# Kernel tuning notes

Measured on AMD Instinct MI355X. Metric: run time of the kernel, lower is better.

## Reference

```python
import jax, jax.numpy as jnp
import numpy as np

HEADS = 8
DIM_HEAD = 64
SCALE = DIM_HEAD ** -0.5


def setup_inputs() -> dict:
    key = jax.random.key(0)
    ks = jax.random.split(key, 5)
    B, N, M, D = 8, 1024, 1024, 512
    inner = HEADS * DIM_HEAD  # 512
    return {
        "x": jax.random.normal(ks[0], (B, N, D), dtype=jnp.float32),
        "context": jax.random.normal(ks[1], (B, M, D), dtype=jnp.float32),
        "Wq": jax.random.normal(ks[2], (D, inner), dtype=jnp.float32) * (D ** -0.5),
        "Wkv": jax.random.normal(ks[3], (D, 2 * inner), dtype=jnp.float32) * (D ** -0.5),
        "Wo": jax.random.normal(ks[4], (inner, D), dtype=jnp.float32) * (inner ** -0.5),
        "bo": jnp.zeros((D,), dtype=jnp.float32),
    }


def reference(x, context, Wq, Wkv, Wo, bo):
    B, N, D = x.shape
    M = context.shape[1]
    q = x @ Wq                      # [B, N, inner]
    kv = context @ Wkv              # [B, M, 2*inner]
    k, v = jnp.split(kv, 2, axis=-1)
    # b n (h d) -> b h n d
    split_heads = lambda t: t.reshape(t.shape[0], t.shape[1], HEADS, DIM_HEAD).transpose(0, 2, 1, 3)
    q, k, v = split_heads(q), split_heads(k), split_heads(v)
    dots = jnp.einsum('bhid,bhjd->bhij', q, k) * SCALE  # [B, H, N, M]
    attn = jax.nn.softmax(dots, axis=-1)
    out = jnp.einsum('bhij,bhjd->bhid', attn, v)        # [B, H, N, d]
    out = out.transpose(0, 2, 1, 3).reshape(B, N, HEADS * DIM_HEAD)
    return out @ Wo + bo            # [B, N, D]
```

## Files before the change

### kernel.cpp

```cpp
#include <hip/hip_runtime.h>
#include <stdint.h>

#define LOG2E 1.44269504088896340736f
#define QSCALE (0.125f * LOG2E)

typedef __bf16 bf16x8 __attribute__((ext_vector_type(8)));
typedef float floatx4 __attribute__((ext_vector_type(4)));

__device__ __forceinline__ unsigned short bfbits(float f) {
  __bf16 h = (__bf16)f;
  return __builtin_bit_cast(unsigned short, h);
}

__device__ __forceinline__ float fast_exp2(float x) {
#if __has_builtin(__builtin_amdgcn_exp2f)
  return __builtin_amdgcn_exp2f(x);
#else
  return exp2f(x);
#endif
}

__device__ __forceinline__ void gl2lds16(const void* g, void* l) {
  __builtin_amdgcn_global_load_lds((const __attribute__((address_space(1))) void*)g,
                                   (__attribute__((address_space(3))) void*)l, 16, 0, 0);
}

__global__ __launch_bounds__(256)
void prep_kernel(const float* __restrict__ x, const float* __restrict__ ctx,
                 const float* __restrict__ Wq, const float* __restrict__ Wkv,
                 const float* __restrict__ Wo,
                 unsigned short* __restrict__ Xb, unsigned short* __restrict__ Cb,
                 unsigned short* __restrict__ WqT, unsigned short* __restrict__ WkvT,
                 unsigned short* __restrict__ WoT) {
  int blk = blockIdx.x;
  int tid = threadIdx.x;
  if (blk < 8192) {
    const float* in = blk < 4096 ? x : ctx;
    unsigned short* out = blk < 4096 ? Xb : Cb;
    int i = (((blk & 4095) * 256) + tid) * 4;
    float4 v = *(const float4*)(in + i);
    unsigned long long pk = (unsigned long long)bfbits(v.x)
                          | ((unsigned long long)bfbits(v.y) << 16)
                          | ((unsigned long long)bfbits(v.z) << 32)
                          | ((unsigned long long)bfbits(v.w) << 48);
    *(unsigned long long*)(out + i) = pk;
  } else {
    __shared__ float tile[32][33];
    int t = blk - 8192;
    const float* in; unsigned short* out; int N; int tb;
    if (t < 256)      { in = Wq;  out = WqT;  N = 512;  tb = t; }
    else if (t < 768) { in = Wkv; out = WkvT; N = 1024; tb = t - 256; }
    else              { in = Wo;  out = WoT;  N = 512;  tb = t - 768; }
    const int K = 512;
    int nbx = N / 32;
    int n0 = (tb % nbx) * 32, k0 = (tb / nbx) * 32;
    int tx = tid & 31, ty = tid >> 5;
#pragma unroll
    for (int r = ty; r < 32; r += 8)
      tile[r][tx] = in[(long)(k0 + r) * N + n0 + tx];
    __syncthreads();
#pragma unroll
    for (int r = ty; r < 32; r += 8)
      out[(long)(n0 + r) * K + k0 + tx] = bfbits(tile[tx][r]);
  }
}

__global__ __launch_bounds__(256)
void proj_gemm(const unsigned short* __restrict__ Xb, const unsigned short* __restrict__ Cb,
               const unsigned short* __restrict__ WqT, const unsigned short* __restrict__ WkvT,
               unsigned short* __restrict__ Qb, unsigned short* __restrict__ Kb,
               unsigned short* __restrict__ Vt) {
  __shared__ unsigned short As[128 * 32];
  __shared__ unsigned short Bs[128 * 32];

  int idx = blockIdx.x;
  const unsigned short* A; const unsigned short* Bt;
  long bm, bn; int role;
  if (idx < 256) { role = 0; A = Xb; Bt = WqT;  bn = (long)(idx & 3) * 128; bm = (long)(idx >> 2) * 128; }
  else { idx -= 256; role = 1; A = Cb; Bt = WkvT; bn = (long)(idx & 7) * 128; bm = (long)(idx >> 3) * 128; }

  const int tid = threadIdx.x;
  const int wave = tid >> 6;
  const int lane = tid & 63;
  const int l15 = lane & 15;
  const int q4 = lane >> 4;
  const int wm = (wave & 1) * 64;
  const int wn = (wave >> 1) * 64;
  const int K = 512;

  floatx4 acc[4][4];
#pragma unroll
  for (int i = 0; i < 4; ++i)
#pragma unroll
    for (int j = 0; j < 4; ++j) { acc[i][j][0]=0.f; acc[i][j][1]=0.f; acc[i][j][2]=0.f; acc[i][j][3]=0.f; }

  for (int k0 = 0; k0 < K; k0 += 32) {
#pragma unroll
    for (int cc = 0; cc < 2; ++cc) {
      int c = cc * 256 + tid;
      int r = c >> 2, kc = c & 3;
      gl2lds16(A + (bm + r) * (long)K + k0 + kc * 8, (char*)As + c * 16);
      gl2lds16(Bt + (bn + r) * (long)K + k0 + kc * 8, (char*)Bs + c * 16);
    }
    __syncthreads();
    bf16x8 af[4], bfr[4];
#pragma unroll
    for (int i = 0; i < 4; ++i)
      af[i] = *(const bf16x8*)(As + (wm + i * 16 + l15) * 32 + q4 * 8);
#pragma unroll
    for (int j = 0; j < 4; ++j)
      bfr[j] = *(const bf16x8*)(Bs + (wn + j * 16 + l15) * 32 + q4 * 8);
#pragma unroll
    for (int i = 0; i < 4; ++i)
#pragma unroll
      for (int j = 0; j < 4; ++j)
        acc[i][j] = __builtin_amdgcn_mfma_f32_16x16x32_bf16(af[i], bfr[j], acc[i][j], 0, 0, 0);
    __syncthreads();
  }

  const bool vrole = (role == 1) && (bn >= 512);
#pragma unroll
  for (int i = 0; i < 4; ++i) {
#pragma unroll
    for (int j = 0; j < 4; ++j) {
      long col = bn + wn + j * 16 + l15;
      if (vrole) {
        long h = (col - 512) >> 6, d = col & 63;
        long row0 = bm + wm + i * 16 + q4 * 4;
        long b = row0 >> 10, m0 = row0 & 1023;
        unsigned long long pk = (unsigned long long)bfbits(acc[i][j][0])
                              | ((unsigned long long)bfbits(acc[i][j][1]) << 16)
                              | ((unsigned long long)bfbits(acc[i][j][2]) << 32)
                              | ((unsigned long long)bfbits(acc[i][j][3]) << 48);
        *(unsigned long long*)(Vt + ((b * 8 + h) * 64 + d) * 1024 + m0) = pk;
      } else {
        long h = col >> 6, d = col & 63;
#pragma unroll
        for (int r = 0; r < 4; ++r) {
          long row = bm + wm + i * 16 + q4 * 4 + r;
          long b = row >> 10, n = row & 1023;
          float v = acc[i][j][r];
          if (role == 0) Qb[((b * 8 + h) * 1024 + n) * 64 + d] = bfbits(v * QSCALE);
          else           Kb[((b * 8 + h) * 1024 + n) * 64 + d] = bfbits(v);
        }
      }
    }
  }
}

__global__ __launch_bounds__(256)
void attn_kernel(const unsigned short* __restrict__ Qb,
                 const unsigned short* __restrict__ Kb,
                 const unsigned short* __restrict__ Vt,
                 unsigned short* __restrict__ Ob)
{
  __shared__ unsigned short Ksm[2][4096];
  __shared__ unsigned short Vsm[2][4096];
  __shared__ unsigned short Psm[128 * 64];

  const int tid = threadIdx.x;
  const int wave = tid >> 6;
  const int lane = tid & 63;
  const int l15 = lane & 15;
  const int q4 = lane >> 4;
  const int bh = blockIdx.x;
  const int nb = blockIdx.y;

  const long qrow0 = (long)bh * 1024 + nb * 128 + wave * 32;

  bf16x8 qf[2][2];
#pragma unroll
  for (int qn = 0; qn < 2; ++qn)
#pragma unroll
    for (int ks = 0; ks < 2; ++ks)
      qf[qn][ks] = *(const bf16x8*)(Qb + (qrow0 + qn * 16 + l15) * 64 + ks * 32 + q4 * 8);

  floatx4 acc[2][4];
#pragma unroll
  for (int i = 0; i < 2; ++i)
#pragma unroll
    for (int d = 0; d < 4; ++d) { acc[i][d][0]=0.f; acc[i][d][1]=0.f; acc[i][d][2]=0.f; acc[i][d][3]=0.f; }
  float suml[2] = {0.0f, 0.0f};

  const unsigned short* Kbase = Kb + (long)bh * 65536;
  const unsigned short* Vbase = Vt + (long)bh * 65536;
  int koff[2], voff[2], lds16[2];
#pragma unroll
  for (int cc = 0; cc < 2; ++cc) {
    int c = cc * 256 + tid;
    int jrow = c >> 3;
    int cact = (c & 7) ^ (jrow & 7);
    koff[cc] = jrow * 64 + cact * 8;
    voff[cc] = jrow * 1024 + cact * 8;
    lds16[cc] = c * 16;
  }
#pragma unroll
  for (int cc = 0; cc < 2; ++cc) {
    gl2lds16(Kbase + koff[cc], (char*)Ksm[0] + lds16[cc]);
    gl2lds16(Vbase + voff[cc], (char*)Vsm[0] + lds16[cc]);
  }

  for (int t = 0; t < 16; ++t) {
    __syncthreads();
    const int cur = t & 1;
    if (t + 1 < 16) {
      const int nxt = cur ^ 1;
#pragma unroll
      for (int cc = 0; cc < 2; ++cc) {
        gl2lds16(Kbase + (t + 1) * 4096 + koff[cc], (char*)Ksm[nxt] + lds16[cc]);
        gl2lds16(Vbase + (t + 1) * 64 + voff[cc], (char*)Vsm[nxt] + lds16[cc]);
      }
    }

    floatx4 st[4][2];
#pragma unroll
    for (int jn = 0; jn < 4; ++jn)
#pragma unroll
      for (int qn = 0; qn < 2; ++qn) { st[jn][qn][0]=0.f; st[jn][qn][1]=0.f; st[jn][qn][2]=0.f; st[jn][qn][3]=0.f; }
#pragma unroll
    for (int ks = 0; ks < 2; ++ks) {
      bf16x8 kfr[4];
#pragma unroll
      for (int jn = 0; jn < 4; ++jn) {
        int j = jn * 16 + l15;
        int cact = (ks * 4 + q4) ^ (j & 7);
        kfr[jn] = *(const bf16x8*)(Ksm[cur] + j * 64 + cact * 8);
      }
#pragma unroll
      for (int jn = 0; jn < 4; ++jn)
#pragma unroll
        for (int qn = 0; qn < 2; ++qn)
          st[jn][qn] = __builtin_amdgcn_mfma_f32_16x16x32_bf16(kfr[jn], qf[qn][ks], st[jn][qn], 0, 0, 0);
    }

#pragma unroll
    for (int qn = 0; qn < 2; ++qn) {
      int prow = wave * 32 + qn * 16 + l15;
#pragma unroll
      for (int jn = 0; jn < 4; ++jn) {
        float p0 = fast_exp2(st[jn][qn][0]);
        float p1 = fast_exp2(st[jn][qn][1]);
        float p2 = fast_exp2(st[jn][qn][2]);
        float p3 = fast_exp2(st[jn][qn][3]);
        suml[qn] += (p0 + p1) + (p2 + p3);
        unsigned long long pk = (unsigned long long)bfbits(p0)
                              | ((unsigned long long)bfbits(p1) << 16)
                              | ((unsigned long long)bfbits(p2) << 32)
                              | ((unsigned long long)bfbits(p3) << 48);
        int ch16 = (jn * 2 + (q4 >> 1)) ^ (prow & 7);
        *(unsigned long long*)(Psm + prow * 64 + ch16 * 8 + (q4 & 1) * 4) = pk;
      }
    }
    __asm__ volatile("s_waitcnt lgkmcnt(0)" ::: "memory");

#pragma unroll
    for (int ks = 0; ks < 2; ++ks) {
      bf16x8 pa[2], vb[4];
#pragma unroll
      for (int i = 0; i < 2; ++i) {
        int m = wave * 32 + i * 16 + l15;
        int cact = (ks * 4 + q4) ^ (m & 7);
        pa[i] = *(const bf16x8*)(Psm + m * 64 + cact * 8);
      }
#pragma unroll
      for (int dn = 0; dn < 4; ++dn) {
        int dd = dn * 16 + l15;
        int cact = (ks * 4 + q4) ^ (dd & 7);
        vb[dn] = *(const bf16x8*)(Vsm[cur] + dd * 64 + cact * 8);
      }
#pragma unroll
      for (int i = 0; i < 2; ++i)
#pragma unroll
        for (int dn = 0; dn < 4; ++dn)
          acc[i][dn] = __builtin_amdgcn_mfma_f32_16x16x32_bf16(pa[i], vb[dn], acc[i][dn], 0, 0, 0);
    }
  }

  float inv[2], invr[2][4];
#pragma unroll
  for (int qn = 0; qn < 2; ++qn) {
    float l = suml[qn];
    l += __shfl_xor(l, 16, 64);
    l += __shfl_xor(l, 32, 64);
    inv[qn] = 1.0f / l;
#pragma unroll
    for (int r = 0; r < 4; ++r) invr[qn][r] = __shfl(inv[qn], q4 * 4 + r, 64);
  }

  const int b = bh >> 3, h = bh & 7;
#pragma unroll
  for (int i = 0; i < 2; ++i) {
#pragma unroll
    for (int dn = 0; dn < 4; ++dn) {
#pragma unroll
      for (int r = 0; r < 4; ++r) {
        long row = (long)b * 1024 + nb * 128 + wave * 32 + i * 16 + q4 * 4 + r;
        long col = h * 64 + dn * 16 + l15;
        Ob[row * 512 + col] = bfbits(acc[i][dn][r] * invr[i][r]);
      }
    }
  }
}

__global__ __launch_bounds__(256)
void out_gemm(const unsigned short* __restrict__ A,
              const unsigned short* __restrict__ Bt,
              float* __restrict__ outF, const float* __restrict__ bias) {
  __shared__ unsigned short As[64 * 32];
  __shared__ unsigned short Bs[128 * 32];

  const int tid = threadIdx.x;
  const int wave = tid >> 6;
  const int lane = tid & 63;
  const int l15 = lane & 15;
  const int q4 = lane >> 4;
  const int wm = (wave & 1) * 32;
  const int wn = (wave >> 1) * 64;
  const long bm = (long)blockIdx.y * 64;
  const long bn = (long)blockIdx.x * 128;
  const int K = 512, N = 512;

  floatx4 acc[2][4];
#pragma unroll
  for (int i = 0; i < 2; ++i)
#pragma unroll
    for (int j = 0; j < 4; ++j) { acc[i][j][0]=0.f; acc[i][j][1]=0.f; acc[i][j][2]=0.f; acc[i][j][3]=0.f; }

  for (int k0 = 0; k0 < K; k0 += 32) {
    {
      int r = tid >> 2, kc = tid & 3;
      gl2lds16(A + (bm + r) * (long)K + k0 + kc * 8, (char*)As + tid * 16);
    }
#pragma unroll
    for (int cc = 0; cc < 2; ++cc) {
      int c = cc * 256 + tid;
      int r = c >> 2, kc = c & 3;
      gl2lds16(Bt + (bn + r) * (long)K + k0 + kc * 8, (char*)Bs + c * 16);
    }
    __syncthreads();
    bf16x8 af[2], bfr[4];
#pragma unroll
    for (int i = 0; i < 2; ++i)
      af[i] = *(const bf16x8*)(As + (wm + i * 16 + l15) * 32 + q4 * 8);
#pragma unroll
    for (int j = 0; j < 4; ++j)
      bfr[j] = *(const bf16x8*)(Bs + (wn + j * 16 + l15) * 32 + q4 * 8);
#pragma unroll
    for (int i = 0; i < 2; ++i)
#pragma unroll
      for (int j = 0; j < 4; ++j)
        acc[i][j] = __builtin_amdgcn_mfma_f32_16x16x32_bf16(af[i], bfr[j], acc[i][j], 0, 0, 0);
    __syncthreads();
  }

#pragma unroll
  for (int i = 0; i < 2; ++i) {
#pragma unroll
    for (int j = 0; j < 4; ++j) {
      long col = bn + wn + j * 16 + l15;
      float bv = bias[col];
#pragma unroll
      for (int r = 0; r < 4; ++r) {
        long row = bm + wm + i * 16 + q4 * 4 + r;
        outF[row * (long)N + col] = acc[i][j][r] + bv;
      }
    }
  }
}

extern "C" void kernel_launch(void* const* d_in, const int* in_sizes, int n_in,
                              void* d_out, int out_size, void* d_ws, size_t ws_size,
                              hipStream_t stream) {
  const float* x   = (const float*)d_in[0];
  const float* ctx = (const float*)d_in[1];
  const float* Wq  = (const float*)d_in[2];
  const float* Wkv = (const float*)d_in[3];
  const float* Wo  = (const float*)d_in[4];
  const float* bo  = (const float*)d_in[5];
  float* out = (float*)d_out;

  char* ws = (char*)d_ws;
  unsigned short* Xb   = (unsigned short*)(ws);
  unsigned short* Cb   = (unsigned short*)(ws + (8u  << 20));
  unsigned short* WqT  = (unsigned short*)(ws + (16u << 20));
  unsigned short* WkvT = (unsigned short*)(ws + (17u << 20));
  unsigned short* WoT  = (unsigned short*)(ws + (19u << 20));
  unsigned short* Qb   = (unsigned short*)(ws + (20u << 20));
  unsigned short* Kb   = (unsigned short*)(ws + (28u << 20));
  unsigned short* Vt   = (unsigned short*)(ws + (36u << 20));
  unsigned short* Ob   = (unsigned short*)(ws + (44u << 20));

  prep_kernel<<<9216, 256, 0, stream>>>(x, ctx, Wq, Wkv, Wo, Xb, Cb, WqT, WkvT, WoT);
  proj_gemm<<<768, 256, 0, stream>>>(Xb, Cb, WqT, WkvT, Qb, Kb, Vt);
  attn_kernel<<<dim3(64, 8), 256, 0, stream>>>(Qb, Kb, Vt, Ob);
  out_gemm<<<dim3(4, 128), 256, 0, stream>>>(Ob, WoT, out, bo);
}
```

Measured before the change: 156.1 us.

## Split attention over key dimension into two partitions with combine kernel

Splits the key/value sequence of the attention kernel into two halves across a new grid z dimension, doubling the block count from 512 to 1024 to better fill the GPU's compute units. Each half writes unnormalized fp32 partial outputs and row sums, and a new combine kernel sums the halves, normalizes, and emits bf16. The P staging buffer is halved by processing the softmax/PV step in two phases, and launch bounds request 4 blocks per unit to raise occupancy. This adds an extra kernel launch and about 32MB of fp32 partial-output traffic. Summing the halves without a max is valid only because the kernel already omits max subtraction.

```diff
diff --git a/kernel.cpp b/kernel.cpp
--- a/kernel.cpp
+++ b/kernel.cpp
@@ -148,15 +148,16 @@
   }
 }
 
-__global__ __launch_bounds__(256)
+__global__ __launch_bounds__(256, 4)
 void attn_kernel(const unsigned short* __restrict__ Qb,
                  const unsigned short* __restrict__ Kb,
                  const unsigned short* __restrict__ Vt,
-                 unsigned short* __restrict__ Ob)
+                 float* __restrict__ Opart,
+                 float* __restrict__ Lpart)
 {
   __shared__ unsigned short Ksm[2][4096];
   __shared__ unsigned short Vsm[2][4096];
-  __shared__ unsigned short Psm[128 * 64];
+  __shared__ unsigned short Psm[128 * 32];
 
   const int tid = threadIdx.x;
   const int wave = tid >> 6;
@@ -165,6 +166,7 @@
   const int q4 = lane >> 4;
   const int bh = blockIdx.x;
   const int nb = blockIdx.y;
+  const int sp = blockIdx.z;
 
   const long qrow0 = (long)bh * 1024 + nb * 128 + wave * 32;
 
@@ -182,8 +184,8 @@
     for (int d = 0; d < 4; ++d) { acc[i][d][0]=0.f; acc[i][d][1]=0.f; acc[i][d][2]=0.f; acc[i][d][3]=0.f; }
   float suml[2] = {0.0f, 0.0f};
 
-  const unsigned short* Kbase = Kb + (long)bh * 65536;
-  const unsigned short* Vbase = Vt + (long)bh * 65536;
+  const unsigned short* Kbase = Kb + (long)bh * 65536 + sp * 8 * 4096;
+  const unsigned short* Vbase = Vt + (long)bh * 65536 + sp * 8 * 64;
   int koff[2], voff[2], lds16[2];
 #pragma unroll
   for (int cc = 0; cc < 2; ++cc) {
@@ -200,10 +202,10 @@
     gl2lds16(Vbase + voff[cc], (char*)Vsm[0] + lds16[cc]);
   }
 
-  for (int t = 0; t < 16; ++t) {
+  for (int t = 0; t < 8; ++t) {
     __syncthreads();
     const int cur = t & 1;
-    if (t + 1 < 16) {
+    if (t + 1 < 8) {
       const int nxt = cur ^ 1;
 #pragma unroll
       for (int cc = 0; cc < 2; ++cc) {
@@ -234,38 +236,39 @@
     }
 
 #pragma unroll
-    for (int qn = 0; qn < 2; ++qn) {
-      int prow = wave * 32 + qn * 16 + l15;
-#pragma unroll
-      for (int jn = 0; jn < 4; ++jn) {
-        float p0 = fast_exp2(st[jn][qn][0]);
-        float p1 = fast_exp2(st[jn][qn][1]);
-        float p2 = fast_exp2(st[jn][qn][2]);
-        float p3 = fast_exp2(st[jn][qn][3]);
-        suml[qn] += (p0 + p1) + (p2 + p3);
-        unsigned long long pk = (unsigned long long)bfbits(p0)
-                              | ((unsigned long long)bfbits(p1) << 16)
-                              | ((unsigned long long)bfbits(p2) << 32)
-                              | ((unsigned long long)bfbits(p3) << 48);
-        int ch16 = (jn * 2 + (q4 >> 1)) ^ (prow & 7);
-        *(unsigned long long*)(Psm + prow * 64 + ch16 * 8 + (q4 & 1) * 4) = pk;
-      }
-    }
-    __asm__ volatile("s_waitcnt lgkmcnt(0)" ::: "memory");
-
-#pragma unroll
-    for (int ks = 0; ks < 2; ++ks) {
+    for (int ph = 0; ph < 2; ++ph) {
+#pragma unroll
+      for (int qn = 0; qn < 2; ++qn) {
+        int prow = wave * 32 + qn * 16 + l15;
+#pragma unroll
+        for (int jj = 0; jj < 2; ++jj) {
+          int jn = ph * 2 + jj;
+          float p0 = fast_exp2(st[jn][qn][0]);
+          float p1 = fast_exp2(st[jn][qn][1]);
+          float p2 = fast_exp2(st[jn][qn][2]);
+          float p3 = fast_exp2(st[jn][qn][3]);
+          suml[qn] += (p0 + p1) + (p2 + p3);
+          unsigned long long pk = (unsigned long long)bfbits(p0)
+                                | ((unsigned long long)bfbits(p1) << 16)
+                                | ((unsigned long long)bfbits(p2) << 32)
+                                | ((unsigned long long)bfbits(p3) << 48);
+          int ch = (jj * 2 + (q4 >> 1)) ^ (prow & 3);
+          *(unsigned long long*)(Psm + prow * 32 + ch * 8 + (q4 & 1) * 4) = pk;
+        }
+      }
+      __asm__ volatile("s_waitcnt lgkmcnt(0)" ::: "memory");
+
       bf16x8 pa[2], vb[4];
 #pragma unroll
       for (int i = 0; i < 2; ++i) {
         int m = wave * 32 + i * 16 + l15;
-        int cact = (ks * 4 + q4) ^ (m & 7);
-        pa[i] = *(const bf16x8*)(Psm + m * 64 + cact * 8);
+        int cact = q4 ^ (m & 3);
+        pa[i] = *(const bf16x8*)(Psm + m * 32 + cact * 8);
       }
 #pragma unroll
       for (int dn = 0; dn < 4; ++dn) {
         int dd = dn * 16 + l15;
-        int cact = (ks * 4 + q4) ^ (dd & 7);
+        int cact = (ph * 4 + q4) ^ (dd & 7);
         vb[dn] = *(const bf16x8*)(Vsm[cur] + dd * 64 + cact * 8);
       }
 #pragma unroll
@@ -276,17 +279,16 @@
     }
   }
 
-  float inv[2], invr[2][4];
 #pragma unroll
   for (int qn = 0; qn < 2; ++qn) {
     float l = suml[qn];
     l += __shfl_xor(l, 16, 64);
     l += __shfl_xor(l, 32, 64);
-    inv[qn] = 1.0f / l;
-#pragma unroll
-    for (int r = 0; r < 4; ++r) invr[qn][r] = __shfl(inv[qn], q4 * 4 + r, 64);
-  }
-
+    if (q4 == 0)
+      Lpart[(long)sp * 65536 + (long)bh * 1024 + nb * 128 + wave * 32 + qn * 16 + l15] = l;
+  }
+
+  float* Op = Opart + (long)sp * 8192 * 512;
   const int b = bh >> 3, h = bh & 7;
 #pragma unroll
   for (int i = 0; i < 2; ++i) {
@@ -296,10 +298,31 @@
       for (int r = 0; r < 4; ++r) {
         long row = (long)b * 1024 + nb * 128 + wave * 32 + i * 16 + q4 * 4 + r;
         long col = h * 64 + dn * 16 + l15;
-        Ob[row * 512 + col] = bfbits(acc[i][dn][r] * invr[i][r]);
-      }
-    }
-  }
+        Op[row * 512 + col] = acc[i][dn][r];
+      }
+    }
+  }
+}
+
+__global__ __launch_bounds__(256)
+void combine_kernel(const float* __restrict__ Opart, const float* __restrict__ Lpart,
+                    unsigned short* __restrict__ Ob) {
+  int g = blockIdx.x * 256 + threadIdx.x;
+  int row = g >> 7;
+  int c4 = g & 127;
+  int b = row >> 10, n = row & 1023, h = c4 >> 4;
+  long lidx = (long)(b * 8 + h) * 1024 + n;
+  float l1 = Lpart[lidx];
+  float l2 = Lpart[65536 + lidx];
+  float inv = 1.0f / (l1 + l2);
+  long oidx = (long)row * 512 + c4 * 4;
+  float4 o1 = *(const float4*)(Opart + oidx);
+  float4 o2 = *(const float4*)(Opart + 8192L * 512 + oidx);
+  unsigned long long pk = (unsigned long long)bfbits((o1.x + o2.x) * inv)
+                        | ((unsigned long long)bfbits((o1.y + o2.y) * inv) << 16)
+                        | ((unsigned long long)bfbits((o1.z + o2.z) * inv) << 32)
+                        | ((unsigned long long)bfbits((o1.w + o2.w) * inv) << 48);
+  *(unsigned long long*)(Ob + oidx) = pk;
 }
 
 __global__ __launch_bounds__(256)
@@ -389,9 +412,12 @@
   unsigned short* Kb   = (unsigned short*)(ws + (28u << 20));
   unsigned short* Vt   = (unsigned short*)(ws + (36u << 20));
   unsigned short* Ob   = (unsigned short*)(ws + (44u << 20));
+  float*          Opart = (float*)(ws + (52u << 20));
+  float*          Lpart = (float*)(ws + (86u << 20));
 
   prep_kernel<<<9216, 256, 0, stream>>>(x, ctx, Wq, Wkv, Wo, Xb, Cb, WqT, WkvT, WoT);
   proj_gemm<<<768, 256, 0, stream>>>(Xb, Cb, WqT, WkvT, Qb, Kb, Vt);
-  attn_kernel<<<dim3(64, 8), 256, 0, stream>>>(Qb, Kb, Vt, Ob);
+  attn_kernel<<<dim3(64, 8, 2), 256, 0, stream>>>(Qb, Kb, Vt, Opart, Lpart);
+  combine_kernel<<<4096, 256, 0, stream>>>(Opart, Lpart, Ob);
   out_gemm<<<dim3(4, 128), 256, 0, stream>>>(Ob, WoT, out, bo);
 }
```

After: 160.7 us. +2.9%, slower.

## Software-pipeline attention loop: defer PV MFMA by one tile, overlapping with exp

Applied to the files above, without the earlier changes.

The attention inner loop now computes P·V for the previous key tile while computing exp and P stores for the current tile. To support this it triple-buffers V in LDS and double-buffers P, and adds an epilogue for the last tile. The goal is to hide the exp/pack latency and the LDS round-trip wait behind MFMA work instead of serializing them with an explicit lgkmcnt wait. Swizzled LDS offsets are also precomputed once. The cost is more LDS per block, which may reduce occupancy, and more live registers.

```diff
diff --git a/kernel.cpp b/kernel.cpp
--- a/kernel.cpp
+++ b/kernel.cpp
@@ -155,8 +155,8 @@
                  unsigned short* __restrict__ Ob)
 {
   __shared__ unsigned short Ksm[2][4096];
-  __shared__ unsigned short Vsm[2][4096];
-  __shared__ unsigned short Psm[128 * 64];
+  __shared__ unsigned short Vsm[3][4096];
+  __shared__ unsigned short Psm[2][8192];
 
   const int tid = threadIdx.x;
   const int wave = tid >> 6;
@@ -194,6 +194,24 @@
     voff[cc] = jrow * 1024 + cact * 8;
     lds16[cc] = c * 16;
   }
+
+  const int s7 = l15 & 7;
+  int kfo[2][4], pao[2][2], pwo[2][4];
+#pragma unroll
+  for (int ks = 0; ks < 2; ++ks) {
+#pragma unroll
+    for (int jn = 0; jn < 4; ++jn)
+      kfo[ks][jn] = (jn * 16 + l15) * 64 + (((ks * 4 + q4) ^ s7) * 8);
+#pragma unroll
+    for (int i = 0; i < 2; ++i)
+      pao[ks][i] = (wave * 32 + i * 16 + l15) * 64 + (((ks * 4 + q4) ^ s7) * 8);
+  }
+#pragma unroll
+  for (int qn = 0; qn < 2; ++qn)
+#pragma unroll
+    for (int jn = 0; jn < 4; ++jn)
+      pwo[qn][jn] = (wave * 32 + qn * 16 + l15) * 64 + (((jn * 2 + (q4 >> 1)) ^ s7) * 8) + (q4 & 1) * 4;
+
 #pragma unroll
   for (int cc = 0; cc < 2; ++cc) {
     gl2lds16(Kbase + koff[cc], (char*)Ksm[0] + lds16[cc]);
@@ -202,13 +220,16 @@
 
   for (int t = 0; t < 16; ++t) {
     __syncthreads();
-    const int cur = t & 1;
+    const int kc = t & 1;
     if (t + 1 < 16) {
-      const int nxt = cur ^ 1;
+      char* KL = (char*)Ksm[kc ^ 1];
+      char* VL = (char*)Vsm[(t + 1) % 3];
+      const unsigned short* Kn = Kbase + (t + 1) * 4096;
+      const unsigned short* Vn = Vbase + (t + 1) * 64;
 #pragma unroll
       for (int cc = 0; cc < 2; ++cc) {
-        gl2lds16(Kbase + (t + 1) * 4096 + koff[cc], (char*)Ksm[nxt] + lds16[cc]);
-        gl2lds16(Vbase + (t + 1) * 64 + voff[cc], (char*)Vsm[nxt] + lds16[cc]);
+        gl2lds16(Kn + koff[cc], KL + lds16[cc]);
+        gl2lds16(Vn + voff[cc], VL + lds16[cc]);
       }
     }
 
@@ -217,15 +238,13 @@
     for (int jn = 0; jn < 4; ++jn)
 #pragma unroll
       for (int qn = 0; qn < 2; ++qn) { st[jn][qn][0]=0.f; st[jn][qn][1]=0.f; st[jn][qn][2]=0.f; st[jn][qn][3]=0.f; }
+    const unsigned short* Kc = Ksm[kc];
 #pragma unroll
     for (int ks = 0; ks < 2; ++ks) {
       bf16x8 kfr[4];
 #pragma unroll
-      for (int jn = 0; jn < 4; ++jn) {
-        int j = jn * 16 + l15;
-        int cact = (ks * 4 + q4) ^ (j & 7);
-        kfr[jn] = *(const bf16x8*)(Ksm[cur] + j * 64 + cact * 8);
-      }
+      for (int jn = 0; jn < 4; ++jn)
+        kfr[jn] = *(const bf16x8*)(Kc + kfo[ks][jn]);
 #pragma unroll
       for (int jn = 0; jn < 4; ++jn)
 #pragma unroll
@@ -233,41 +252,76 @@
           st[jn][qn] = __builtin_amdgcn_mfma_f32_16x16x32_bf16(kfr[jn], qf[qn][ks], st[jn][qn], 0, 0, 0);
     }
 
-#pragma unroll
-    for (int qn = 0; qn < 2; ++qn) {
-      int prow = wave * 32 + qn * 16 + l15;
-#pragma unroll
-      for (int jn = 0; jn < 4; ++jn) {
-        float p0 = fast_exp2(st[jn][qn][0]);
-        float p1 = fast_exp2(st[jn][qn][1]);
-        float p2 = fast_exp2(st[jn][qn][2]);
-        float p3 = fast_exp2(st[jn][qn][3]);
-        suml[qn] += (p0 + p1) + (p2 + p3);
-        unsigned long long pk = (unsigned long long)bfbits(p0)
-                              | ((unsigned long long)bfbits(p1) << 16)
-                              | ((unsigned long long)bfbits(p2) << 32)
-                              | ((unsigned long long)bfbits(p3) << 48);
-        int ch16 = (jn * 2 + (q4 >> 1)) ^ (prow & 7);
-        *(unsigned long long*)(Psm + prow * 64 + ch16 * 8 + (q4 & 1) * 4) = pk;
-      }
-    }
-    __asm__ volatile("s_waitcnt lgkmcnt(0)" ::: "memory");
-
+    unsigned short* Pc = Psm[t & 1];
+    const unsigned short* Pp = Psm[(t & 1) ^ 1];
+    const unsigned short* Vp = Vsm[(t + 2) % 3];
+    const bool havePrev = (t > 0);
+
+    bf16x8 pa0[2], vb0[4];
+    if (havePrev) {
+#pragma unroll
+      for (int i = 0; i < 2; ++i) pa0[i] = *(const bf16x8*)(Pp + pao[0][i]);
+#pragma unroll
+      for (int dn = 0; dn < 4; ++dn) vb0[dn] = *(const bf16x8*)(Vp + kfo[0][dn]);
+    }
+#pragma unroll
+    for (int jn = 0; jn < 4; ++jn) {
+      float p0 = fast_exp2(st[jn][0][0]);
+      float p1 = fast_exp2(st[jn][0][1]);
+      float p2 = fast_exp2(st[jn][0][2]);
+      float p3 = fast_exp2(st[jn][0][3]);
+      suml[0] += (p0 + p1) + (p2 + p3);
+      unsigned int lo = (unsigned int)bfbits(p0) | ((unsigned int)bfbits(p1) << 16);
+      unsigned int hi = (unsigned int)bfbits(p2) | ((unsigned int)bfbits(p3) << 16);
+      unsigned long long pk = (unsigned long long)lo | ((unsigned long long)hi << 32);
+      *(unsigned long long*)(Pc + pwo[0][jn]) = pk;
+    }
+    if (havePrev) {
+#pragma unroll
+      for (int i = 0; i < 2; ++i)
+#pragma unroll
+        for (int dn = 0; dn < 4; ++dn)
+          acc[i][dn] = __builtin_amdgcn_mfma_f32_16x16x32_bf16(pa0[i], vb0[dn], acc[i][dn], 0, 0, 0);
+    }
+
+    bf16x8 pa1[2], vb1[4];
+    if (havePrev) {
+#pragma unroll
+      for (int i = 0; i < 2; ++i) pa1[i] = *(const bf16x8*)(Pp + pao[1][i]);
+#pragma unroll
+      for (int dn = 0; dn < 4; ++dn) vb1[dn] = *(const bf16x8*)(Vp + kfo[1][dn]);
+    }
+#pragma unroll
+    for (int jn = 0; jn < 4; ++jn) {
+      float p0 = fast_exp2(st[jn][1][0]);
+      float p1 = fast_exp2(st[jn][1][1]);
+      float p2 = fast_exp2(st[jn][1][2]);
+      float p3 = fast_exp2(st[jn][1][3]);
+      suml[1] += (p0 + p1) + (p2 + p3);
+      unsigned int lo = (unsigned int)bfbits(p0) | ((unsigned int)bfbits(p1) << 16);
+      unsigned int hi = (unsigned int)bfbits(p2) | ((unsigned int)bfbits(p3) << 16);
+      unsigned long long pk = (unsigned long long)lo | ((unsigned long long)hi << 32);
+      *(unsigned long long*)(Pc + pwo[1][jn]) = pk;
+    }
+    if (havePrev) {
+#pragma unroll
+      for (int i = 0; i < 2; ++i)
+#pragma unroll
+        for (int dn = 0; dn < 4; ++dn)
+          acc[i][dn] = __builtin_amdgcn_mfma_f32_16x16x32_bf16(pa1[i], vb1[dn], acc[i][dn], 0, 0, 0);
+    }
+  }
+
+  {
+    const unsigned short* Pp = Psm[1];
+    const unsigned short* Vp = Vsm[15 % 3];
 #pragma unroll
     for (int ks = 0; ks < 2; ++ks) {
       bf16x8 pa[2], vb[4];
 #pragma unroll
-      for (int i = 0; i < 2; ++i) {
-        int m = wave * 32 + i * 16 + l15;
-        int cact = (ks * 4 + q4) ^ (m & 7);
-        pa[i] = *(const bf16x8*)(Psm + m * 64 + cact * 8);
-      }
-#pragma unroll
-      for (int dn = 0; dn < 4; ++dn) {
-        int dd = dn * 16 + l15;
-        int cact = (ks * 4 + q4) ^ (dd & 7);
-        vb[dn] = *(const bf16x8*)(Vsm[cur] + dd * 64 + cact * 8);
-      }
+      for (int i = 0; i < 2; ++i) pa[i] = *(const bf16x8*)(Pp + pao[ks][i]);
+#pragma unroll
+      for (int dn = 0; dn < 4; ++dn) vb[dn] = *(const bf16x8*)(Vp + kfo[ks][dn]);
 #pragma unroll
       for (int i = 0; i < 2; ++i)
 #pragma unroll
```

Measured after the change: 156.6 us. No clear change (+0.3%).

## Double KV tile to 128 keys per iteration and precompute LDS offsets

Applied to the files above, without the earlier changes.

The attention inner loop now handles 128 keys per step instead of 64, halving the iteration count and the number of block barriers. K and V LDS buffers double in size, and V uses a 16-way XOR swizzle to match the wider rows. P is written and consumed in two 64-key phases so the P buffer stays the same size. Fragment and store offsets are hoisted into precomputed arrays. This raises LDS use to about 80KB per block and adds register pressure from 16 score accumulators, which may lower occupancy.

```diff
diff --git a/kernel.cpp b/kernel.cpp
--- a/kernel.cpp
+++ b/kernel.cpp
@@ -154,9 +154,9 @@
                  const unsigned short* __restrict__ Vt,
                  unsigned short* __restrict__ Ob)
 {
-  __shared__ unsigned short Ksm[2][4096];
-  __shared__ unsigned short Vsm[2][4096];
-  __shared__ unsigned short Psm[128 * 64];
+  __shared__ unsigned short Ksm[2][8192];
+  __shared__ unsigned short Vsm[2][8192];
+  __shared__ unsigned short Psm[8192];
 
   const int tid = threadIdx.x;
   const int wave = tid >> 6;
@@ -184,95 +184,122 @@
 
   const unsigned short* Kbase = Kb + (long)bh * 65536;
   const unsigned short* Vbase = Vt + (long)bh * 65536;
-  int koff[2], voff[2], lds16[2];
-#pragma unroll
-  for (int cc = 0; cc < 2; ++cc) {
+  int koff[4], voff[4], lds16[4];
+#pragma unroll
+  for (int cc = 0; cc < 4; ++cc) {
     int c = cc * 256 + tid;
-    int jrow = c >> 3;
-    int cact = (c & 7) ^ (jrow & 7);
-    koff[cc] = jrow * 64 + cact * 8;
-    voff[cc] = jrow * 1024 + cact * 8;
+    int kr = c >> 3;
+    int kcact = (c & 7) ^ (kr & 7);
+    koff[cc] = kr * 64 + kcact * 8;
+    int vr = c >> 4;
+    int vcact = (c & 15) ^ (vr & 15);
+    voff[cc] = vr * 1024 + vcact * 8;
     lds16[cc] = c * 16;
   }
-#pragma unroll
-  for (int cc = 0; cc < 2; ++cc) {
+
+  const int s7 = l15 & 7;
+  int kfo[2][8];
+#pragma unroll
+  for (int ks = 0; ks < 2; ++ks)
+#pragma unroll
+    for (int jn = 0; jn < 8; ++jn)
+      kfo[ks][jn] = (jn * 16 + l15) * 64 + (((ks * 4 + q4) ^ s7) * 8);
+  int vfo[2][2][4];
+#pragma unroll
+  for (int ph = 0; ph < 2; ++ph)
+#pragma unroll
+    for (int ks = 0; ks < 2; ++ks)
+#pragma unroll
+      for (int dn = 0; dn < 4; ++dn) {
+        int r = dn * 16 + l15;
+        vfo[ph][ks][dn] = r * 128 + (((ph * 8 + ks * 4 + q4) ^ (r & 15)) * 8);
+      }
+  int pao[2][2], pwo[2][4];
+#pragma unroll
+  for (int ks = 0; ks < 2; ++ks)
+#pragma unroll
+    for (int i = 0; i < 2; ++i)
+      pao[ks][i] = (wave * 32 + i * 16 + l15) * 64 + (((ks * 4 + q4) ^ s7) * 8);
+#pragma unroll
+  for (int qn = 0; qn < 2; ++qn)
+#pragma unroll
+    for (int jl = 0; jl < 4; ++jl)
+      pwo[qn][jl] = (wave * 32 + qn * 16 + l15) * 64 + (((jl * 2 + (q4 >> 1)) ^ s7) * 8) + (q4 & 1) * 4;
+
+#pragma unroll
+  for (int cc = 0; cc < 4; ++cc) {
     gl2lds16(Kbase + koff[cc], (char*)Ksm[0] + lds16[cc]);
     gl2lds16(Vbase + voff[cc], (char*)Vsm[0] + lds16[cc]);
   }
 
-  for (int t = 0; t < 16; ++t) {
+  for (int t = 0; t < 8; ++t) {
     __syncthreads();
     const int cur = t & 1;
-    if (t + 1 < 16) {
+    if (t + 1 < 8) {
       const int nxt = cur ^ 1;
-#pragma unroll
-      for (int cc = 0; cc < 2; ++cc) {
-        gl2lds16(Kbase + (t + 1) * 4096 + koff[cc], (char*)Ksm[nxt] + lds16[cc]);
-        gl2lds16(Vbase + (t + 1) * 64 + voff[cc], (char*)Vsm[nxt] + lds16[cc]);
-      }
-    }
-
-    floatx4 st[4][2];
-#pragma unroll
-    for (int jn = 0; jn < 4; ++jn)
+      const unsigned short* Kn = Kbase + (t + 1) * 8192;
+      const unsigned short* Vn = Vbase + (t + 1) * 128;
+#pragma unroll
+      for (int cc = 0; cc < 4; ++cc) {
+        gl2lds16(Kn + koff[cc], (char*)Ksm[nxt] + lds16[cc]);
+        gl2lds16(Vn + voff[cc], (char*)Vsm[nxt] + lds16[cc]);
+      }
+    }
+
+    floatx4 st[8][2];
+#pragma unroll
+    for (int jn = 0; jn < 8; ++jn)
 #pragma unroll
       for (int qn = 0; qn < 2; ++qn) { st[jn][qn][0]=0.f; st[jn][qn][1]=0.f; st[jn][qn][2]=0.f; st[jn][qn][3]=0.f; }
+    const unsigned short* Kc = Ksm[cur];
 #pragma unroll
     for (int ks = 0; ks < 2; ++ks) {
-      bf16x8 kfr[4];
-#pragma unroll
-      for (int jn = 0; jn < 4; ++jn) {
-        int j = jn * 16 + l15;
-        int cact = (ks * 4 + q4) ^ (j & 7);
-        kfr[jn] = *(const bf16x8*)(Ksm[cur] + j * 64 + cact * 8);
-      }
-#pragma unroll
-      for (int jn = 0; jn < 4; ++jn)
+      bf16x8 kfr[8];
+#pragma unroll
+      for (int jn = 0; jn < 8; ++jn)
+        kfr[jn] = *(const bf16x8*)(Kc + kfo[ks][jn]);
+#pragma unroll
+      for (int jn = 0; jn < 8; ++jn)
 #pragma unroll
         for (int qn = 0; qn < 2; ++qn)
           st[jn][qn] = __builtin_amdgcn_mfma_f32_16x16x32_bf16(kfr[jn], qf[qn][ks], st[jn][qn], 0, 0, 0);
     }
 
-#pragma unroll
-    for (int qn = 0; qn < 2; ++qn) {
-      int prow = wave * 32 + qn * 16 + l15;
-#pragma unroll
-      for (int jn = 0; jn < 4; ++jn) {
-        float p0 = fast_exp2(st[jn][qn][0]);
-        float p1 = fast_exp2(st[jn][qn][1]);
-        float p2 = fast_exp2(st[jn][qn][2]);
-        float p3 = fast_exp2(st[jn][qn][3]);
-        suml[qn] += (p0 + p1) + (p2 + p3);
-        unsigned long long pk = (unsigned long long)bfbits(p0)
-                              | ((unsigned long long)bfbits(p1) << 16)
-                              | ((unsigned long long)bfbits(p2) << 32)
-                              | ((unsigned long long)bfbits(p3) << 48);
-        int ch16 = (jn * 2 + (q4 >> 1)) ^ (prow & 7);
-        *(unsigned long long*)(Psm + prow * 64 + ch16 * 8 + (q4 & 1) * 4) = pk;
-      }
-    }
-    __asm__ volatile("s_waitcnt lgkmcnt(0)" ::: "memory");
-
-#pragma unroll
-    for (int ks = 0; ks < 2; ++ks) {
-      bf16x8 pa[2], vb[4];
-#pragma unroll
-      for (int i = 0; i < 2; ++i) {
-        int m = wave * 32 + i * 16 + l15;
-        int cact = (ks * 4 + q4) ^ (m & 7);
-        pa[i] = *(const bf16x8*)(Psm + m * 64 + cact * 8);
-      }
-#pragma unroll
-      for (int dn = 0; dn < 4; ++dn) {
-        int dd = dn * 16 + l15;
-        int cact = (ks * 4 + q4) ^ (dd & 7);
-        vb[dn] = *(const bf16x8*)(Vsm[cur] + dd * 64 + cact * 8);
-      }
-#pragma unroll
-      for (int i = 0; i < 2; ++i)
+    const unsigned short* Vc = Vsm[cur];
+#pragma unroll
+    for (int ph = 0; ph < 2; ++ph) {
+#pragma unroll
+      for (int qn = 0; qn < 2; ++qn) {
+#pragma unroll
+        for (int jl = 0; jl < 4; ++jl) {
+          int jn = ph * 4 + jl;
+          float p0 = fast_exp2(st[jn][qn][0]);
+          float p1 = fast_exp2(st[jn][qn][1]);
+          float p2 = fast_exp2(st[jn][qn][2]);
+          float p3 = fast_exp2(st[jn][qn][3]);
+          suml[qn] += (p0 + p1) + (p2 + p3);
+          unsigned int lo = (unsigned int)bfbits(p0) | ((unsigned int)bfbits(p1) << 16);
+          unsigned int hi = (unsigned int)bfbits(p2) | ((unsigned int)bfbits(p3) << 16);
+          unsigned long long pk = (unsigned long long)lo | ((unsigned long long)hi << 32);
+          *(unsigned long long*)(Psm + pwo[qn][jl]) = pk;
+        }
+      }
+      __asm__ volatile("s_waitcnt lgkmcnt(0)" ::: "memory");
+#pragma unroll
+      for (int ks = 0; ks < 2; ++ks) {
+        bf16x8 pa[2], vb[4];
+#pragma unroll
+        for (int i = 0; i < 2; ++i)
+          pa[i] = *(const bf16x8*)(Psm + pao[ks][i]);
 #pragma unroll
         for (int dn = 0; dn < 4; ++dn)
-          acc[i][dn] = __builtin_amdgcn_mfma_f32_16x16x32_bf16(pa[i], vb[dn], acc[i][dn], 0, 0, 0);
+          vb[dn] = *(const bf16x8*)(Vc + vfo[ph][ks][dn]);
+#pragma unroll
+        for (int i = 0; i < 2; ++i)
+#pragma unroll
+          for (int dn = 0; dn < 4; ++dn)
+            acc[i][dn] = __builtin_amdgcn_mfma_f32_16x16x32_bf16(pa[i], vb[dn], acc[i][dn], 0, 0, 0);
+      }
     }
   }
 
```

Result: no change. 154.9 us (-0.8%).
